# Kernel tuning notes

Measured on AMD Instinct MI355X. Metric: run time of the kernel, lower is better.

The kernel has to match this reference:

```python
import jax, jax.numpy as jnp
import numpy as np

SEQ_LEN, BATCH, HID, INP = 512, 256, 256, 256


def setup_inputs() -> dict:
    key = jax.random.key(0)
    ks = jax.random.split(key, 6)
    s = 1.0 / np.sqrt(HID)  # torch GRUCell init scale
    return {
        "carry": jnp.zeros((BATCH, HID), jnp.float32),
        "seq_inputs": jax.random.normal(ks[0], (SEQ_LEN, BATCH, INP), jnp.float32),
        "seq_resets": jax.random.randint(ks[1], (SEQ_LEN, BATCH), 0, 2, jnp.int32),
        "w_ih": jax.random.uniform(ks[2], (3 * HID, INP), jnp.float32, -s, s),
        "w_hh": jax.random.uniform(ks[3], (3 * HID, HID), jnp.float32, -s, s),
        "b_ih": jax.random.uniform(ks[4], (3 * HID,), jnp.float32, -s, s),
        "b_hh": jax.random.uniform(ks[5], (3 * HID,), jnp.float32, -s, s),
    }


def reference(carry, seq_inputs, seq_resets, w_ih, w_hh, b_ih, b_hh):
    # Precompute the input-side projection for all timesteps in one GEMM.
    gi_all = jnp.einsum('tbi,gi->tbg', seq_inputs, w_ih) + b_ih  # (T,B,3H)

    def step(h, xs):
        gi, reset_t = xs
        h = jnp.where(reset_t[:, None] > 0, jnp.zeros_like(h), h)
        gh = h @ w_hh.T + b_hh  # (B,3H)
        i_r, i_z, i_n = jnp.split(gi, 3, axis=1)
        h_r, h_z, h_n = jnp.split(gh, 3, axis=1)
        r = jax.nn.sigmoid(i_r + h_r)
        z = jax.nn.sigmoid(i_z + h_z)
        n = jnp.tanh(i_n + r * h_n)
        h_new = (1.0 - z) * n + z * h
        return h_new, h_new

    h_final, outputs = jax.lax.scan(step, carry, (gi_all, seq_resets))
    return h_final, outputs
```

## Files before the change

kernel.cpp:

```cpp
#include <hip/hip_runtime.h>
#include <hip/hip_bf16.h>
#include <hip/hip_fp16.h>


#define T_LEN 512
#define BATCH 256
#define HID   256

typedef __attribute__((ext_vector_type(8))) short s16x8;
typedef __attribute__((ext_vector_type(8))) unsigned short u16x8;
typedef __attribute__((ext_vector_type(4))) float fx4;

#define MFMA16 __builtin_amdgcn_mfma_f32_16x16x32_bf16
#define GATE_STRIDE 4096u
#define BLK_STRIDE  12288u
#define T_STRIDE    196608u

__device__ __forceinline__ unsigned short f2bf(float f) {
  union { float f; unsigned u; } v; v.f = f;
  unsigned r = v.u + 0x7fffu + ((v.u >> 16) & 1u);
  return (unsigned short)(r >> 16);
}

__device__ __forceinline__ unsigned cvt_pk_bf16(float lo, float hi) {
  unsigned r;
  asm("v_cvt_pk_bf16_f32 %0, %1, %2" : "=v"(r) : "v"(lo), "v"(hi));
  return r;
}

__device__ __forceinline__ s16x8 pack8(float4 a, float4 b) {
  s16x8 f;
  f[0] = (short)f2bf(a.x); f[1] = (short)f2bf(a.y);
  f[2] = (short)f2bf(a.z); f[3] = (short)f2bf(a.w);
  f[4] = (short)f2bf(b.x); f[5] = (short)f2bf(b.y);
  f[6] = (short)f2bf(b.z); f[7] = (short)f2bf(b.w);
  return f;
}

__device__ __forceinline__ s16x8 pack8i(float4 a, float4 b) {
  s16x8 f;
  f[0] = (short)f2bf(a.x); f[1] = (short)f2bf(b.x);
  f[2] = (short)f2bf(a.y); f[3] = (short)f2bf(b.y);
  f[4] = (short)f2bf(a.z); f[5] = (short)f2bf(b.z);
  f[6] = (short)f2bf(a.w); f[7] = (short)f2bf(b.w);
  return f;
}

template<bool SIGMA>
__device__ __forceinline__ void load_weights(const float* __restrict__ W,
                                             s16x8 (&wr)[4][8], char* Wlds,
                                             int tid, int wid, int col, int kgrp) {
#pragma unroll
  for (int g = 0; g < 2; ++g)
#pragma unroll
    for (int ht = 0; ht < 2; ++ht) {
      int row = g * 256 + (wid * 2 + ht) * 16 + col;
#pragma unroll
      for (int s8 = 0; s8 < 8; ++s8) {
        if (SIGMA) {
          const float* pa = W + row * 256 + s8 * 32 + kgrp * 4;
          wr[g * 2 + ht][s8] = pack8i(*(const float4*)pa, *(const float4*)(pa + 16));
        } else {
          const float* pa = W + row * 256 + s8 * 32 + kgrp * 8;
          wr[g * 2 + ht][s8] = pack8(*(const float4*)pa, *(const float4*)(pa + 4));
        }
      }
    }
#pragma unroll
  for (int q = 0; q < 16; ++q) {
    int li = tid + q * 512;
    int wv = li >> 9, s8 = (li >> 6) & 7, l = li & 63;
    int row = 512 + wv * 16 + (l & 15);
    s16x8 line;
    if (SIGMA) {
      const float* pa = W + row * 256 + s8 * 32 + (l >> 4) * 4;
      line = pack8i(*(const float4*)pa, *(const float4*)(pa + 16));
    } else {
      const float* pa = W + row * 256 + s8 * 32 + (l >> 4) * 8;
      line = pack8(*(const float4*)pa, *(const float4*)(pa + 4));
    }
    *(s16x8*)(Wlds + li * 16) = line;
  }
}

__device__ __forceinline__ void soft_barrier() {
  asm volatile("s_waitcnt lgkmcnt(0)" ::: "memory");
  __builtin_amdgcn_s_barrier();
  __builtin_amdgcn_sched_barrier(0);
  asm volatile("" ::: "memory");
}

__global__ __launch_bounds__(512, 2) void gi_proj_kernel(
    const float* __restrict__ X, const float* __restrict__ w_ih,
    const float* __restrict__ b_ih, const float* __restrict__ b_hh,
    __half* __restrict__ gi) {
  __shared__ __align__(16) char Wlds[131072];
  __shared__ __align__(16) char Ald[2][8192];

  const int tid = threadIdx.x;
  const int wid = tid >> 6, lane = tid & 63;
  const int col = lane & 15, kgrp = lane >> 4;

  s16x8 wr[4][8];
  load_weights<false>(w_ih, wr, Wlds, tid, wid, col, kgrp);

  float bias[2][3];
#pragma unroll
  for (int ht = 0; ht < 2; ++ht) {
    int gb = (wid * 2 + ht) * 16 + col;
    bias[ht][0] = b_ih[gb]       + b_hh[gb];
    bias[ht][1] = b_ih[256 + gb] + b_hh[256 + gb];
    bias[ht][2] = b_ih[512 + gb];
  }

  const int srow = tid >> 5, sk = (tid & 31) * 8;
  const unsigned sbyte = ((unsigned)(srow * 512 + sk * 2)) ^ ((unsigned)(srow & 7) << 4);

  float4 xc0 = *(const float4*)(X + (size_t)(blockIdx.x * 16 + srow) * 256 + sk);
  float4 xc1 = *(const float4*)(X + (size_t)(blockIdx.x * 16 + srow) * 256 + sk + 4);

  int parity = 0;
  for (int chunk = blockIdx.x; chunk < (T_LEN * BATCH) / 16; chunk += 256) {
    char* ab = Ald[parity];
    {
      uint4 v;
      v.x = cvt_pk_bf16(xc0.x, xc0.y);
      v.y = cvt_pk_bf16(xc0.z, xc0.w);
      v.z = cvt_pk_bf16(xc1.x, xc1.y);
      v.w = cvt_pk_bf16(xc1.z, xc1.w);
      *(uint4*)(ab + sbyte) = v;
    }
    int nchunk = chunk + 256;
    if (nchunk < (T_LEN * BATCH) / 16) {
      xc0 = *(const float4*)(X + (size_t)(nchunk * 16 + srow) * 256 + sk);
      xc1 = *(const float4*)(X + (size_t)(nchunk * 16 + srow) * 256 + sk + 4);
    }
    soft_barrier();

    fx4 a00, a10, a01, a11, a02, a12;
#pragma unroll
    for (int j = 0; j < 4; ++j) {
      a00[j] = bias[0][0]; a10[j] = bias[1][0];
      a01[j] = bias[0][1]; a11[j] = bias[1][1];
      a02[j] = bias[0][2]; a12[j] = bias[1][2];
    }

#pragma unroll
    for (int s8 = 0; s8 < 8; ++s8) {
      unsigned aoff = ((unsigned)(col * 512 + (s8 * 32 + kgrp * 8) * 2)) ^
                      ((unsigned)(col & 7) << 4);
      s16x8 af  = *(const s16x8*)(ab + aoff);
      s16x8 w2a = *(const s16x8*)(Wlds + (((wid * 2 + 0) * 8 + s8) * 64 + lane) * 16);
      s16x8 w2b = *(const s16x8*)(Wlds + (((wid * 2 + 1) * 8 + s8) * 64 + lane) * 16);
      a00 = MFMA16(af, wr[0][s8], a00, 0, 0, 0);
      a10 = MFMA16(af, wr[1][s8], a10, 0, 0, 0);
      a01 = MFMA16(af, wr[2][s8], a01, 0, 0, 0);
      a11 = MFMA16(af, wr[3][s8], a11, 0, 0, 0);
      a02 = MFMA16(af, w2a, a02, 0, 0, 0);
      a12 = MFMA16(af, w2b, a12, 0, 0, 0);
    }

    __half* gb = gi + (size_t)chunk * BLK_STRIDE + (unsigned)(wid * 64 + lane) * 8;
    u16x8 o0, o1, o2;
#pragma unroll
    for (int j = 0; j < 4; ++j) {
      o0[j] = __half_as_ushort(__float2half(a00[j]));
      o0[4 + j] = __half_as_ushort(__float2half(a10[j]));
      o1[j] = __half_as_ushort(__float2half(a01[j]));
      o1[4 + j] = __half_as_ushort(__float2half(a11[j]));
      o2[j] = __half_as_ushort(__float2half(a02[j]));
      o2[4 + j] = __half_as_ushort(__float2half(a12[j]));
    }
    *(u16x8*)(gb) = o0;
    *(u16x8*)(gb + GATE_STRIDE) = o1;
    *(u16x8*)(gb + 2 * GATE_STRIDE) = o2;
    parity ^= 1;
  }
}

__global__ __launch_bounds__(512, 2) void gru_scan_kernel(
    const float* __restrict__ carry, const __half* __restrict__ gi,
    const int* __restrict__ resets, const float* __restrict__ w_hh,
    const float* __restrict__ b_hh, float* __restrict__ out) {
  __shared__ __align__(16) char Wlds[131072];
  __shared__ __align__(16) char Ald[2][8192];
  __shared__ int lastreset[16];

  const int tid = threadIdx.x;
  const int wid = tid >> 6, lane = tid & 63;
  const int col = lane & 15, kgrp = lane >> 4;
  const int bid = blockIdx.x;
  const int bt = bid & 15, c = bid >> 4;
  const int b0 = bt * 16, t0 = c * 32, t1 = t0 + 32;
  const int hid0 = wid * 32 + col;

  s16x8 wr[4][8];
  load_weights<true>(w_hh, wr, Wlds, tid, wid, col, kgrp);
  const float bhhn0 = b_hh[512 + hid0], bhhn1 = b_hh[512 + hid0 + 16];

  int s, useCarry;
  if (c == 0) {
    s = 0; useCarry = 1;
  } else {
    if (tid < 16) lastreset[tid] = -1;
    for (int base = t0 - 32;; base -= 32) {
      __syncthreads();
      int tt = base + (tid >> 4);
      if (tt >= 0 && tt < t0) {
        if (resets[tt * BATCH + b0 + (tid & 15)] != 0)
          atomicMax(&lastreset[tid & 15], tt);
      }
      __syncthreads();
      int mn = t0, all = 1;
#pragma unroll
      for (int i = 0; i < 16; ++i) {
        int v = lastreset[i];
        all &= (v >= 0) ? 1 : 0;
        mn = min(mn, v < 0 ? t0 : v);
      }
      if (all) { s = mn; useCarry = 0; break; }
      if (base <= 0) { s = 0; useCarry = 1; break; }
    }
  }

  {
    int row = tid >> 5, k0 = (tid & 31) * 8;
    int tile = k0 >> 5, colb = (k0 >> 1) & 15;
    int rst = resets[s * BATCH + b0 + row];
    float4 va = {0.f, 0.f, 0.f, 0.f}, vb = va;
    if (useCarry && !rst) {
      va = *(const float4*)(carry + (size_t)(b0 + row) * HID + tile * 32 + colb);
      vb = *(const float4*)(carry + (size_t)(b0 + row) * HID + tile * 32 + colb + 16);
    }
    uint4 u;
    u.x = cvt_pk_bf16(va.x, vb.x);
    u.y = cvt_pk_bf16(va.y, vb.y);
    u.z = cvt_pk_bf16(va.z, vb.z);
    u.w = cvt_pk_bf16(va.w, vb.w);
    unsigned byteoff = ((unsigned)(row * 512 + k0 * 2)) ^ ((unsigned)(row & 7) << 4);
    *(uint4*)(Ald[0] + byteoff) = u;
  }
  float hprev[2][4];
#pragma unroll
  for (int ht = 0; ht < 2; ++ht)
#pragma unroll
    for (int j = 0; j < 4; ++j) {
      int b = kgrp * 4 + j;
      int rst = resets[s * BATCH + b0 + b];
      float hv = 0.f;
      if (useCarry && !rst) hv = carry[(size_t)(b0 + b) * HID + hid0 + ht * 16];
      hprev[ht][j] = hv;
    }
  __syncthreads();

  const __half* gp = gi + (size_t)(s * 16 + bt) * BLK_STRIDE + (unsigned)(wid * 64 + lane) * 8;
  const int* rbase = resets + b0 + kgrp * 4;
  float* opc = out + 65536 + ((size_t)s * BATCH + b0 + kgrp * 4) * HID + hid0;

  u16x8 gP0 = *(const u16x8*)(gp);
  u16x8 gP1 = *(const u16x8*)(gp + GATE_STRIDE);
  u16x8 gP2 = *(const u16x8*)(gp + 2 * GATE_STRIDE);
  int4 rnC = *(const int4*)(rbase + (size_t)((s + 1 < T_LEN) ? s + 1 : T_LEN - 1) * BATCH);

  for (int t = s; t < t1; ++t) {
    const __half* gq = gp + ((t + 1 < t1) ? T_STRIDE : 0u);
    u16x8 gN0 = *(const u16x8*)(gq);
    u16x8 gN1 = *(const u16x8*)(gq + GATE_STRIDE);
    u16x8 gN2 = *(const u16x8*)(gq + 2 * GATE_STRIDE);
    int tn = (t + 2 < T_LEN) ? t + 2 : T_LEN - 1;
    int4 rnN = *(const int4*)(rbase + (size_t)tn * BATCH);

    fx4 a00, a10, a01, a11, a02, a12;
#pragma unroll
    for (int j = 0; j < 4; ++j) {
      a00[j] = __half2float(__ushort_as_half(gP0[j]));
      a10[j] = __half2float(__ushort_as_half(gP0[4 + j]));
      a01[j] = __half2float(__ushort_as_half(gP1[j]));
      a11[j] = __half2float(__ushort_as_half(gP1[4 + j]));
      a02[j] = bhhn0;
      a12[j] = bhhn1;
    }

    const char* ab = Ald[(t - s) & 1];
#pragma unroll
    for (int s8 = 0; s8 < 8; ++s8) {
      unsigned aoff = ((unsigned)(col * 512 + (s8 * 32 + kgrp * 8) * 2)) ^
                      ((unsigned)(col & 7) << 4);
      s16x8 af  = *(const s16x8*)(ab + aoff);
      s16x8 w2a = *(const s16x8*)(Wlds + (((wid * 2 + 0) * 8 + s8) * 64 + lane) * 16);
      s16x8 w2b = *(const s16x8*)(Wlds + (((wid * 2 + 1) * 8 + s8) * 64 + lane) * 16);
      a00 = MFMA16(af, wr[0][s8], a00, 0, 0, 0);
      a10 = MFMA16(af, wr[1][s8], a10, 0, 0, 0);
      a01 = MFMA16(af, wr[2][s8], a01, 0, 0, 0);
      a11 = MFMA16(af, wr[3][s8], a11, 0, 0, 0);
      a02 = MFMA16(af, w2a, a02, 0, 0, 0);
      a12 = MFMA16(af, w2b, a12, 0, 0, 0);
    }

    char* aw = (char*)Ald[((t - s) & 1) ^ 1];
    const bool wr_out = (t >= t0);
    const bool lastT = (t + 1 >= T_LEN);
#pragma unroll
    for (int j = 0; j < 4; ++j) {
      int b = kgrp * 4 + j;
      int rj = (j == 0) ? rnC.x : (j == 1) ? rnC.y : (j == 2) ? rnC.z : rnC.w;
      if (lastT) rj = 0;

      float r0 = __builtin_amdgcn_rcpf(1.f + __expf(-a00[j]));
      float z0 = __builtin_amdgcn_rcpf(1.f + __expf(-a01[j]));
      float pn0 = __half2float(__ushort_as_half(gP2[j])) + r0 * a02[j];
      float n0 = 1.f - 2.f * __builtin_amdgcn_rcpf(1.f + __expf(2.f * pn0));
      float h0 = (1.f - z0) * n0 + z0 * hprev[0][j];

      float r1 = __builtin_amdgcn_rcpf(1.f + __expf(-a10[j]));
      float z1 = __builtin_amdgcn_rcpf(1.f + __expf(-a11[j]));
      float pn1 = __half2float(__ushort_as_half(gP2[4 + j])) + r1 * a12[j];
      float n1 = 1.f - 2.f * __builtin_amdgcn_rcpf(1.f + __expf(2.f * pn1));
      float h1 = (1.f - z1) * n1 + z1 * hprev[1][j];

      if (wr_out) {
        __builtin_nontemporal_store(h0, opc + j * HID);
        __builtin_nontemporal_store(h1, opc + j * HID + 16);
      }

      float hk0 = rj ? 0.f : h0;
      float hk1 = rj ? 0.f : h1;
      hprev[0][j] = hk0; hprev[1][j] = hk1;

      unsigned hw = cvt_pk_bf16(hk0, hk1);
      unsigned hoff = ((unsigned)(b * 512 + wid * 64 + col * 4)) ^
                      ((unsigned)(b & 7) << 4);
      *(unsigned*)(aw + hoff) = hw;
    }

    gP0 = gN0; gP1 = gN1; gP2 = gN2; rnC = rnN;
    gp = gq;
    opc += 65536;
    soft_barrier();
  }

  if (c == 15) {
#pragma unroll
    for (int ht = 0; ht < 2; ++ht)
#pragma unroll
      for (int j = 0; j < 4; ++j)
        out[(size_t)(b0 + kgrp * 4 + j) * HID + hid0 + ht * 16] = hprev[ht][j];
  }
}

extern "C" void kernel_launch(void* const* d_in, const int* in_sizes, int n_in,
                              void* d_out, int out_size, void* d_ws, size_t ws_size,
                              hipStream_t stream) {
  const float* carry = (const float*)d_in[0];
  const float* X     = (const float*)d_in[1];
  const int*   rsts  = (const int*)d_in[2];
  const float* w_ih  = (const float*)d_in[3];
  const float* w_hh  = (const float*)d_in[4];
  const float* b_ih  = (const float*)d_in[5];
  const float* b_hh  = (const float*)d_in[6];
  float* out = (float*)d_out;

  const size_t gi_bytes = (size_t)T_LEN * BATCH * 3 * HID * sizeof(__half);
  if (ws_size < gi_bytes) return;
  __half* gi = (__half*)d_ws;

  gi_proj_kernel<<<256, 512, 0, stream>>>(X, w_ih, b_ih, b_hh, gi);
  gru_scan_kernel<<<256, 512, 0, stream>>>(carry, gi, rsts, w_hh, b_hh, out);
}
```

Baseline: 247.3 us.

## Process 32 batch rows per block with 16-step chunks and interleaved gate layout

Each GRU scan block now covers 32 batch rows (two M-tiles) over 16-step time chunks instead of 16 rows over 32 steps. That keeps the block count the same while each weight fragment loaded from registers and LDS feeds twice as many MFMAs. The gi projection layout is changed to interleave r/z/n per lane, giving contiguous 48-half loads, and the projection kernel is tiled to match. Shorter chunks reduce the redundant warm-up recompute before each chunk start. The cost is more register pressure (doubled accumulators and prefetched gates) and a larger LDS activation buffer.

```diff
diff --git a/kernel.cpp b/kernel.cpp
--- a/kernel.cpp
+++ b/kernel.cpp
@@ -6,15 +6,15 @@
 #define T_LEN 512
 #define BATCH 256
 #define HID   256
+#define CHL   16
 
 typedef __attribute__((ext_vector_type(8))) short s16x8;
 typedef __attribute__((ext_vector_type(8))) unsigned short u16x8;
 typedef __attribute__((ext_vector_type(4))) float fx4;
 
 #define MFMA16 __builtin_amdgcn_mfma_f32_16x16x32_bf16
-#define GATE_STRIDE 4096u
-#define BLK_STRIDE  12288u
-#define T_STRIDE    196608u
+#define BLKH  24576u
+#define TSTRH 196608u
 
 __device__ __forceinline__ unsigned short f2bf(float f) {
   union { float f; unsigned u; } v; v.f = f;
@@ -48,29 +48,28 @@
 
 template<bool SIGMA>
 __device__ __forceinline__ void load_weights(const float* __restrict__ W,
-                                             s16x8 (&wr)[4][8], char* Wlds,
+                                             s16x8 (&wrA)[4][8], char* Wlds,
                                              int tid, int wid, int col, int kgrp) {
-#pragma unroll
-  for (int g = 0; g < 2; ++g)
-#pragma unroll
-    for (int ht = 0; ht < 2; ++ht) {
-      int row = g * 256 + (wid * 2 + ht) * 16 + col;
-#pragma unroll
-      for (int s8 = 0; s8 < 8; ++s8) {
-        if (SIGMA) {
-          const float* pa = W + row * 256 + s8 * 32 + kgrp * 4;
-          wr[g * 2 + ht][s8] = pack8i(*(const float4*)pa, *(const float4*)(pa + 16));
-        } else {
-          const float* pa = W + row * 256 + s8 * 32 + kgrp * 8;
-          wr[g * 2 + ht][s8] = pack8(*(const float4*)pa, *(const float4*)(pa + 4));
-        }
-      }
-    }
+  const int rowbase[4] = {0, 16, 256, 512};
+#pragma unroll
+  for (int k = 0; k < 4; ++k) {
+    int row = rowbase[k] + wid * 32 + col;
+#pragma unroll
+    for (int s8 = 0; s8 < 8; ++s8) {
+      if (SIGMA) {
+        const float* pa = W + row * 256 + s8 * 32 + kgrp * 4;
+        wrA[k][s8] = pack8i(*(const float4*)pa, *(const float4*)(pa + 16));
+      } else {
+        const float* pa = W + row * 256 + s8 * 32 + kgrp * 8;
+        wrA[k][s8] = pack8(*(const float4*)pa, *(const float4*)(pa + 4));
+      }
+    }
+  }
 #pragma unroll
   for (int q = 0; q < 16; ++q) {
     int li = tid + q * 512;
-    int wv = li >> 9, s8 = (li >> 6) & 7, l = li & 63;
-    int row = 512 + wv * 16 + (l & 15);
+    int set = li >> 12, wv = (li >> 9) & 7, s8 = (li >> 6) & 7, l = li & 63;
+    int row = (set ? 512 : 256) + wv * 32 + 16 + (l & 15);
     s16x8 line;
     if (SIGMA) {
       const float* pa = W + row * 256 + s8 * 32 + (l >> 4) * 4;
@@ -95,85 +94,93 @@
     const float* __restrict__ b_ih, const float* __restrict__ b_hh,
     __half* __restrict__ gi) {
   __shared__ __align__(16) char Wlds[131072];
-  __shared__ __align__(16) char Ald[2][8192];
+  __shared__ __align__(16) char Ald[2][16384];
 
   const int tid = threadIdx.x;
   const int wid = tid >> 6, lane = tid & 63;
   const int col = lane & 15, kgrp = lane >> 4;
 
-  s16x8 wr[4][8];
-  load_weights<false>(w_ih, wr, Wlds, tid, wid, col, kgrp);
+  s16x8 wrA[4][8];
+  load_weights<false>(w_ih, wrA, Wlds, tid, wid, col, kgrp);
 
   float bias[2][3];
 #pragma unroll
   for (int ht = 0; ht < 2; ++ht) {
-    int gb = (wid * 2 + ht) * 16 + col;
+    int gb = wid * 32 + ht * 16 + col;
     bias[ht][0] = b_ih[gb]       + b_hh[gb];
     bias[ht][1] = b_ih[256 + gb] + b_hh[256 + gb];
     bias[ht][2] = b_ih[512 + gb];
   }
 
-  const int srow = tid >> 5, sk = (tid & 31) * 8;
-  const unsigned sbyte = ((unsigned)(srow * 512 + sk * 2)) ^ ((unsigned)(srow & 7) << 4);
-
-  float4 xc0 = *(const float4*)(X + (size_t)(blockIdx.x * 16 + srow) * 256 + sk);
-  float4 xc1 = *(const float4*)(X + (size_t)(blockIdx.x * 16 + srow) * 256 + sk + 4);
+  const int srow = tid >> 4, skb = tid & 15;
+  const unsigned sx = (unsigned)(srow & 7) << 4;
+  const unsigned sb0 = (unsigned)(srow * 512 + skb * 32);
+
+  float4 xc0, xc1, xc2, xc3;
+  {
+    const float* xp = X + (size_t)(blockIdx.x * 32 + srow) * 256 + skb * 16;
+    xc0 = *(const float4*)(xp); xc1 = *(const float4*)(xp + 4);
+    xc2 = *(const float4*)(xp + 8); xc3 = *(const float4*)(xp + 12);
+  }
 
   int parity = 0;
-  for (int chunk = blockIdx.x; chunk < (T_LEN * BATCH) / 16; chunk += 256) {
+  for (int c32 = blockIdx.x; c32 < 4096; c32 += 256) {
     char* ab = Ald[parity];
     {
-      uint4 v;
-      v.x = cvt_pk_bf16(xc0.x, xc0.y);
-      v.y = cvt_pk_bf16(xc0.z, xc0.w);
-      v.z = cvt_pk_bf16(xc1.x, xc1.y);
-      v.w = cvt_pk_bf16(xc1.z, xc1.w);
-      *(uint4*)(ab + sbyte) = v;
-    }
-    int nchunk = chunk + 256;
-    if (nchunk < (T_LEN * BATCH) / 16) {
-      xc0 = *(const float4*)(X + (size_t)(nchunk * 16 + srow) * 256 + sk);
-      xc1 = *(const float4*)(X + (size_t)(nchunk * 16 + srow) * 256 + sk + 4);
+      uint4 u0, u1;
+      u0.x = cvt_pk_bf16(xc0.x, xc0.y); u0.y = cvt_pk_bf16(xc0.z, xc0.w);
+      u0.z = cvt_pk_bf16(xc1.x, xc1.y); u0.w = cvt_pk_bf16(xc1.z, xc1.w);
+      u1.x = cvt_pk_bf16(xc2.x, xc2.y); u1.y = cvt_pk_bf16(xc2.z, xc2.w);
+      u1.z = cvt_pk_bf16(xc3.x, xc3.y); u1.w = cvt_pk_bf16(xc3.z, xc3.w);
+      *(uint4*)(ab + (sb0 ^ sx)) = u0;
+      *(uint4*)(ab + ((sb0 + 16) ^ sx)) = u1;
+    }
+    int nc = c32 + 256;
+    if (nc < 4096) {
+      const float* xp = X + (size_t)(nc * 32 + srow) * 256 + skb * 16;
+      xc0 = *(const float4*)(xp); xc1 = *(const float4*)(xp + 4);
+      xc2 = *(const float4*)(xp + 8); xc3 = *(const float4*)(xp + 12);
     }
     soft_barrier();
 
-    fx4 a00, a10, a01, a11, a02, a12;
-#pragma unroll
-    for (int j = 0; j < 4; ++j) {
-      a00[j] = bias[0][0]; a10[j] = bias[1][0];
-      a01[j] = bias[0][1]; a11[j] = bias[1][1];
-      a02[j] = bias[0][2]; a12[j] = bias[1][2];
-    }
-
-#pragma unroll
-    for (int s8 = 0; s8 < 8; ++s8) {
-      unsigned aoff = ((unsigned)(col * 512 + (s8 * 32 + kgrp * 8) * 2)) ^
-                      ((unsigned)(col & 7) << 4);
-      s16x8 af  = *(const s16x8*)(ab + aoff);
-      s16x8 w2a = *(const s16x8*)(Wlds + (((wid * 2 + 0) * 8 + s8) * 64 + lane) * 16);
-      s16x8 w2b = *(const s16x8*)(Wlds + (((wid * 2 + 1) * 8 + s8) * 64 + lane) * 16);
-      a00 = MFMA16(af, wr[0][s8], a00, 0, 0, 0);
-      a10 = MFMA16(af, wr[1][s8], a10, 0, 0, 0);
-      a01 = MFMA16(af, wr[2][s8], a01, 0, 0, 0);
-      a11 = MFMA16(af, wr[3][s8], a11, 0, 0, 0);
-      a02 = MFMA16(af, w2a, a02, 0, 0, 0);
-      a12 = MFMA16(af, w2b, a12, 0, 0, 0);
-    }
-
-    __half* gb = gi + (size_t)chunk * BLK_STRIDE + (unsigned)(wid * 64 + lane) * 8;
-    u16x8 o0, o1, o2;
-#pragma unroll
-    for (int j = 0; j < 4; ++j) {
-      o0[j] = __half_as_ushort(__float2half(a00[j]));
-      o0[4 + j] = __half_as_ushort(__float2half(a10[j]));
-      o1[j] = __half_as_ushort(__float2half(a01[j]));
-      o1[4 + j] = __half_as_ushort(__float2half(a11[j]));
-      o2[j] = __half_as_ushort(__float2half(a02[j]));
-      o2[4 + j] = __half_as_ushort(__float2half(a12[j]));
-    }
-    *(u16x8*)(gb) = o0;
-    *(u16x8*)(gb + GATE_STRIDE) = o1;
-    *(u16x8*)(gb + 2 * GATE_STRIDE) = o2;
+    __half* gb = gi + (size_t)c32 * BLKH + (unsigned)(wid * 64 + lane) * 48;
+#pragma unroll
+    for (int m = 0; m < 2; ++m) {
+      fx4 aR0, aR1, aZ0, aZ1, aN0, aN1;
+#pragma unroll
+      for (int j = 0; j < 4; ++j) {
+        aR0[j] = bias[0][0]; aR1[j] = bias[1][0];
+        aZ0[j] = bias[0][1]; aZ1[j] = bias[1][1];
+        aN0[j] = bias[0][2]; aN1[j] = bias[1][2];
+      }
+#pragma unroll
+      for (int s8 = 0; s8 < 8; ++s8) {
+        unsigned aoff = ((unsigned)((m * 16 + col) * 512 + s8 * 64 + kgrp * 16)) ^
+                        ((unsigned)(col & 7) << 4);
+        s16x8 af  = *(const s16x8*)(ab + aoff);
+        s16x8 wz1 = *(const s16x8*)(Wlds + (wid * 512 + s8 * 64 + lane) * 16);
+        s16x8 wn1 = *(const s16x8*)(Wlds + 65536 + (wid * 512 + s8 * 64 + lane) * 16);
+        aR0 = MFMA16(af, wrA[0][s8], aR0, 0, 0, 0);
+        aR1 = MFMA16(af, wrA[1][s8], aR1, 0, 0, 0);
+        aZ0 = MFMA16(af, wrA[2][s8], aZ0, 0, 0, 0);
+        aZ1 = MFMA16(af, wz1, aZ1, 0, 0, 0);
+        aN0 = MFMA16(af, wrA[3][s8], aN0, 0, 0, 0);
+        aN1 = MFMA16(af, wn1, aN1, 0, 0, 0);
+      }
+      u16x8 oR, oZ, oN;
+#pragma unroll
+      for (int j = 0; j < 4; ++j) {
+        oR[j] = __half_as_ushort(__float2half(aR0[j]));
+        oR[4 + j] = __half_as_ushort(__float2half(aR1[j]));
+        oZ[j] = __half_as_ushort(__float2half(aZ0[j]));
+        oZ[4 + j] = __half_as_ushort(__float2half(aZ1[j]));
+        oN[j] = __half_as_ushort(__float2half(aN0[j]));
+        oN[4 + j] = __half_as_ushort(__float2half(aN1[j]));
+      }
+      *(u16x8*)(gb + m * 8) = oR;
+      *(u16x8*)(gb + 16 + m * 8) = oZ;
+      *(u16x8*)(gb + 32 + m * 8) = oN;
+    }
     parity ^= 1;
   }
 }
@@ -183,37 +190,37 @@
     const int* __restrict__ resets, const float* __restrict__ w_hh,
     const float* __restrict__ b_hh, float* __restrict__ out) {
   __shared__ __align__(16) char Wlds[131072];
-  __shared__ __align__(16) char Ald[2][8192];
-  __shared__ int lastreset[16];
+  __shared__ __align__(16) char Ald[2][16384];
+  int* lastreset = (int*)(Ald[1]);
 
   const int tid = threadIdx.x;
   const int wid = tid >> 6, lane = tid & 63;
   const int col = lane & 15, kgrp = lane >> 4;
   const int bid = blockIdx.x;
-  const int bt = bid & 15, c = bid >> 4;
-  const int b0 = bt * 16, t0 = c * 32, t1 = t0 + 32;
+  const int bt = bid & 7, c = bid >> 3;
+  const int b0 = bt * 32, t0 = c * CHL, t1 = t0 + CHL;
   const int hid0 = wid * 32 + col;
 
-  s16x8 wr[4][8];
-  load_weights<true>(w_hh, wr, Wlds, tid, wid, col, kgrp);
+  s16x8 wrA[4][8];
+  load_weights<true>(w_hh, wrA, Wlds, tid, wid, col, kgrp);
   const float bhhn0 = b_hh[512 + hid0], bhhn1 = b_hh[512 + hid0 + 16];
 
   int s, useCarry;
   if (c == 0) {
     s = 0; useCarry = 1;
   } else {
-    if (tid < 16) lastreset[tid] = -1;
-    for (int base = t0 - 32;; base -= 32) {
+    if (tid < 32) lastreset[tid] = -1;
+    for (int base = t0 - 16;; base -= 16) {
       __syncthreads();
-      int tt = base + (tid >> 4);
+      int tt = base + (tid >> 5);
       if (tt >= 0 && tt < t0) {
-        if (resets[tt * BATCH + b0 + (tid & 15)] != 0)
-          atomicMax(&lastreset[tid & 15], tt);
+        if (resets[tt * BATCH + b0 + (tid & 31)] != 0)
+          atomicMax(&lastreset[tid & 31], tt);
       }
       __syncthreads();
       int mn = t0, all = 1;
 #pragma unroll
-      for (int i = 0; i < 16; ++i) {
+      for (int i = 0; i < 32; ++i) {
         int v = lastreset[i];
         all &= (v >= 0) ? 1 : 0;
         mn = min(mn, v < 0 ? t0 : v);
@@ -221,130 +228,160 @@
       if (all) { s = mn; useCarry = 0; break; }
       if (base <= 0) { s = 0; useCarry = 1; break; }
     }
+    __syncthreads();
   }
 
   {
-    int row = tid >> 5, k0 = (tid & 31) * 8;
-    int tile = k0 >> 5, colb = (k0 >> 1) & 15;
+    int row = tid >> 4, kblk = tid & 15;
     int rst = resets[s * BATCH + b0 + row];
-    float4 va = {0.f, 0.f, 0.f, 0.f}, vb = va;
+    float4 va0 = {0.f, 0.f, 0.f, 0.f}, va1 = va0, vb0 = va0, vb1 = va0;
     if (useCarry && !rst) {
-      va = *(const float4*)(carry + (size_t)(b0 + row) * HID + tile * 32 + colb);
-      vb = *(const float4*)(carry + (size_t)(b0 + row) * HID + tile * 32 + colb + 16);
-    }
-    uint4 u;
-    u.x = cvt_pk_bf16(va.x, vb.x);
-    u.y = cvt_pk_bf16(va.y, vb.y);
-    u.z = cvt_pk_bf16(va.z, vb.z);
-    u.w = cvt_pk_bf16(va.w, vb.w);
-    unsigned byteoff = ((unsigned)(row * 512 + k0 * 2)) ^ ((unsigned)(row & 7) << 4);
-    *(uint4*)(Ald[0] + byteoff) = u;
-  }
-  float hprev[2][4];
-#pragma unroll
-  for (int ht = 0; ht < 2; ++ht)
+      const float* cp = carry + (size_t)(b0 + row) * HID + (kblk >> 1) * 32 + (kblk & 1) * 8;
+      va0 = *(const float4*)(cp);      va1 = *(const float4*)(cp + 4);
+      vb0 = *(const float4*)(cp + 16); vb1 = *(const float4*)(cp + 20);
+    }
+    uint4 u0, u1;
+    u0.x = cvt_pk_bf16(va0.x, vb0.x); u0.y = cvt_pk_bf16(va0.y, vb0.y);
+    u0.z = cvt_pk_bf16(va0.z, vb0.z); u0.w = cvt_pk_bf16(va0.w, vb0.w);
+    u1.x = cvt_pk_bf16(va1.x, vb1.x); u1.y = cvt_pk_bf16(va1.y, vb1.y);
+    u1.z = cvt_pk_bf16(va1.z, vb1.z); u1.w = cvt_pk_bf16(va1.w, vb1.w);
+    unsigned sx = (unsigned)(row & 7) << 4;
+    unsigned sb0 = (unsigned)(row * 512 + kblk * 32);
+    *(uint4*)(Ald[0] + (sb0 ^ sx)) = u0;
+    *(uint4*)(Ald[0] + ((sb0 + 16) ^ sx)) = u1;
+  }
+  float hprev[2][2][4];
+#pragma unroll
+  for (int m = 0; m < 2; ++m)
 #pragma unroll
     for (int j = 0; j < 4; ++j) {
-      int b = kgrp * 4 + j;
-      int rst = resets[s * BATCH + b0 + b];
-      float hv = 0.f;
-      if (useCarry && !rst) hv = carry[(size_t)(b0 + b) * HID + hid0 + ht * 16];
-      hprev[ht][j] = hv;
-    }
+      int b = b0 + m * 16 + kgrp * 4 + j;
+      int rst = resets[s * BATCH + b];
+      float h0 = 0.f, h1 = 0.f;
+      if (useCarry && !rst) {
+        h0 = carry[(size_t)b * HID + hid0];
+        h1 = carry[(size_t)b * HID + hid0 + 16];
+      }
+      hprev[m][0][j] = h0; hprev[m][1][j] = h1;
+    }
+
+  const __half* gb = gi + (size_t)(s * 8 + bt) * BLKH + (unsigned)(wid * 64 + lane) * 48;
+  u16x8 gC[3][2];
+#pragma unroll
+  for (int g = 0; g < 3; ++g)
+#pragma unroll
+    for (int m = 0; m < 2; ++m)
+      gC[g][m] = *(const u16x8*)(gb + g * 16 + m * 8);
+  int4 rnC[2];
+  {
+    int tn = (s + 1 < T_LEN) ? s + 1 : T_LEN - 1;
+#pragma unroll
+    for (int m = 0; m < 2; ++m)
+      rnC[m] = *(const int4*)(resets + (size_t)tn * BATCH + b0 + m * 16 + kgrp * 4);
+  }
+  float* opc = out + 65536 + ((size_t)s * BATCH + b0 + kgrp * 4) * HID + hid0;
   __syncthreads();
 
-  const __half* gp = gi + (size_t)(s * 16 + bt) * BLK_STRIDE + (unsigned)(wid * 64 + lane) * 8;
-  const int* rbase = resets + b0 + kgrp * 4;
-  float* opc = out + 65536 + ((size_t)s * BATCH + b0 + kgrp * 4) * HID + hid0;
-
-  u16x8 gP0 = *(const u16x8*)(gp);
-  u16x8 gP1 = *(const u16x8*)(gp + GATE_STRIDE);
-  u16x8 gP2 = *(const u16x8*)(gp + 2 * GATE_STRIDE);
-  int4 rnC = *(const int4*)(rbase + (size_t)((s + 1 < T_LEN) ? s + 1 : T_LEN - 1) * BATCH);
-
   for (int t = s; t < t1; ++t) {
-    const __half* gq = gp + ((t + 1 < t1) ? T_STRIDE : 0u);
-    u16x8 gN0 = *(const u16x8*)(gq);
-    u16x8 gN1 = *(const u16x8*)(gq + GATE_STRIDE);
-    u16x8 gN2 = *(const u16x8*)(gq + 2 * GATE_STRIDE);
-    int tn = (t + 2 < T_LEN) ? t + 2 : T_LEN - 1;
-    int4 rnN = *(const int4*)(rbase + (size_t)tn * BATCH);
-
-    fx4 a00, a10, a01, a11, a02, a12;
-#pragma unroll
-    for (int j = 0; j < 4; ++j) {
-      a00[j] = __half2float(__ushort_as_half(gP0[j]));
-      a10[j] = __half2float(__ushort_as_half(gP0[4 + j]));
-      a01[j] = __half2float(__ushort_as_half(gP1[j]));
-      a11[j] = __half2float(__ushort_as_half(gP1[4 + j]));
-      a02[j] = bhhn0;
-      a12[j] = bhhn1;
+    const __half* gq = gb + ((t + 1 < t1) ? TSTRH : 0u);
+    u16x8 gN[3][2];
+#pragma unroll
+    for (int g = 0; g < 3; ++g)
+#pragma unroll
+      for (int m = 0; m < 2; ++m)
+        gN[g][m] = *(const u16x8*)(gq + g * 16 + m * 8);
+    int4 rnN[2];
+    {
+      int tn = (t + 2 < T_LEN) ? t + 2 : T_LEN - 1;
+#pragma unroll
+      for (int m = 0; m < 2; ++m)
+        rnN[m] = *(const int4*)(resets + (size_t)tn * BATCH + b0 + m * 16 + kgrp * 4);
     }
 
     const char* ab = Ald[(t - s) & 1];
-#pragma unroll
-    for (int s8 = 0; s8 < 8; ++s8) {
-      unsigned aoff = ((unsigned)(col * 512 + (s8 * 32 + kgrp * 8) * 2)) ^
-                      ((unsigned)(col & 7) << 4);
-      s16x8 af  = *(const s16x8*)(ab + aoff);
-      s16x8 w2a = *(const s16x8*)(Wlds + (((wid * 2 + 0) * 8 + s8) * 64 + lane) * 16);
-      s16x8 w2b = *(const s16x8*)(Wlds + (((wid * 2 + 1) * 8 + s8) * 64 + lane) * 16);
-      a00 = MFMA16(af, wr[0][s8], a00, 0, 0, 0);
-      a10 = MFMA16(af, wr[1][s8], a10, 0, 0, 0);
-      a01 = MFMA16(af, wr[2][s8], a01, 0, 0, 0);
-      a11 = MFMA16(af, wr[3][s8], a11, 0, 0, 0);
-      a02 = MFMA16(af, w2a, a02, 0, 0, 0);
-      a12 = MFMA16(af, w2b, a12, 0, 0, 0);
-    }
-
     char* aw = (char*)Ald[((t - s) & 1) ^ 1];
-    const bool wr_out = (t >= t0);
     const bool lastT = (t + 1 >= T_LEN);
-#pragma unroll
-    for (int j = 0; j < 4; ++j) {
-      int b = kgrp * 4 + j;
-      int rj = (j == 0) ? rnC.x : (j == 1) ? rnC.y : (j == 2) ? rnC.z : rnC.w;
-      if (lastT) rj = 0;
-
-      float r0 = __builtin_amdgcn_rcpf(1.f + __expf(-a00[j]));
-      float z0 = __builtin_amdgcn_rcpf(1.f + __expf(-a01[j]));
-      float pn0 = __half2float(__ushort_as_half(gP2[j])) + r0 * a02[j];
-      float n0 = 1.f - 2.f * __builtin_amdgcn_rcpf(1.f + __expf(2.f * pn0));
-      float h0 = (1.f - z0) * n0 + z0 * hprev[0][j];
-
-      float r1 = __builtin_amdgcn_rcpf(1.f + __expf(-a10[j]));
-      float z1 = __builtin_amdgcn_rcpf(1.f + __expf(-a11[j]));
-      float pn1 = __half2float(__ushort_as_half(gP2[4 + j])) + r1 * a12[j];
-      float n1 = 1.f - 2.f * __builtin_amdgcn_rcpf(1.f + __expf(2.f * pn1));
-      float h1 = (1.f - z1) * n1 + z1 * hprev[1][j];
-
-      if (wr_out) {
-        __builtin_nontemporal_store(h0, opc + j * HID);
-        __builtin_nontemporal_store(h1, opc + j * HID + 16);
-      }
-
-      float hk0 = rj ? 0.f : h0;
-      float hk1 = rj ? 0.f : h1;
-      hprev[0][j] = hk0; hprev[1][j] = hk1;
-
-      unsigned hw = cvt_pk_bf16(hk0, hk1);
-      unsigned hoff = ((unsigned)(b * 512 + wid * 64 + col * 4)) ^
-                      ((unsigned)(b & 7) << 4);
-      *(unsigned*)(aw + hoff) = hw;
-    }
-
-    gP0 = gN0; gP1 = gN1; gP2 = gN2; rnC = rnN;
-    gp = gq;
+
+#pragma unroll
+    for (int m = 0; m < 2; ++m) {
+      fx4 aR0, aR1, aZ0, aZ1, aN0, aN1;
+#pragma unroll
+      for (int j = 0; j < 4; ++j) {
+        aR0[j] = __half2float(__ushort_as_half(gC[0][m][j]));
+        aR1[j] = __half2float(__ushort_as_half(gC[0][m][4 + j]));
+        aZ0[j] = __half2float(__ushort_as_half(gC[1][m][j]));
+        aZ1[j] = __half2float(__ushort_as_half(gC[1][m][4 + j]));
+        aN0[j] = bhhn0;
+        aN1[j] = bhhn1;
+      }
+#pragma unroll
+      for (int s8 = 0; s8 < 8; ++s8) {
+        unsigned aoff = ((unsigned)((m * 16 + col) * 512 + s8 * 64 + kgrp * 16)) ^
+                        ((unsigned)(col & 7) << 4);
+        s16x8 af  = *(const s16x8*)(ab + aoff);
+        s16x8 wz1 = *(const s16x8*)(Wlds + (wid * 512 + s8 * 64 + lane) * 16);
+        s16x8 wn1 = *(const s16x8*)(Wlds + 65536 + (wid * 512 + s8 * 64 + lane) * 16);
+        aR0 = MFMA16(af, wrA[0][s8], aR0, 0, 0, 0);
+        aR1 = MFMA16(af, wrA[1][s8], aR1, 0, 0, 0);
+        aZ0 = MFMA16(af, wrA[2][s8], aZ0, 0, 0, 0);
+        aZ1 = MFMA16(af, wz1, aZ1, 0, 0, 0);
+        aN0 = MFMA16(af, wrA[3][s8], aN0, 0, 0, 0);
+        aN1 = MFMA16(af, wn1, aN1, 0, 0, 0);
+      }
+
+      int4 rm = rnC[m];
+#pragma unroll
+      for (int j = 0; j < 4; ++j) {
+        int b = m * 16 + kgrp * 4 + j;
+        int rj = (j == 0) ? rm.x : (j == 1) ? rm.y : (j == 2) ? rm.z : rm.w;
+        if (lastT) rj = 0;
+
+        float r0 = __builtin_amdgcn_rcpf(1.f + __expf(-aR0[j]));
+        float z0 = __builtin_amdgcn_rcpf(1.f + __expf(-aZ0[j]));
+        float pn0 = __half2float(__ushort_as_half(gC[2][m][j])) + r0 * aN0[j];
+        float n0 = 1.f - 2.f * __builtin_amdgcn_rcpf(1.f + __expf(2.f * pn0));
+        float h0 = (1.f - z0) * n0 + z0 * hprev[m][0][j];
+
+        float r1 = __builtin_amdgcn_rcpf(1.f + __expf(-aR1[j]));
+        float z1 = __builtin_amdgcn_rcpf(1.f + __expf(-aZ1[j]));
+        float pn1 = __half2float(__ushort_as_half(gC[2][m][4 + j])) + r1 * aN1[j];
+        float n1 = 1.f - 2.f * __builtin_amdgcn_rcpf(1.f + __expf(2.f * pn1));
+        float h1 = (1.f - z1) * n1 + z1 * hprev[m][1][j];
+
+        __builtin_nontemporal_store(h0, opc + m * 4096 + j * HID);
+        __builtin_nontemporal_store(h1, opc + m * 4096 + j * HID + 16);
+
+        float hk0 = rj ? 0.f : h0;
+        float hk1 = rj ? 0.f : h1;
+        hprev[m][0][j] = hk0; hprev[m][1][j] = hk1;
+
+        unsigned hw = cvt_pk_bf16(hk0, hk1);
+        unsigned hoff = ((unsigned)(b * 512 + wid * 64 + col * 4)) ^
+                        ((unsigned)(b & 7) << 4);
+        *(unsigned*)(aw + hoff) = hw;
+      }
+    }
+
+#pragma unroll
+    for (int g = 0; g < 3; ++g)
+#pragma unroll
+      for (int m = 0; m < 2; ++m)
+        gC[g][m] = gN[g][m];
+    rnC[0] = rnN[0]; rnC[1] = rnN[1];
+    gb = gq;
     opc += 65536;
     soft_barrier();
   }
 
-  if (c == 15) {
-#pragma unroll
-    for (int ht = 0; ht < 2; ++ht)
-#pragma unroll
-      for (int j = 0; j < 4; ++j)
-        out[(size_t)(b0 + kgrp * 4 + j) * HID + hid0 + ht * 16] = hprev[ht][j];
+  if (c == 31) {
+#pragma unroll
+    for (int m = 0; m < 2; ++m)
+#pragma unroll
+      for (int j = 0; j < 4; ++j) {
+        int b = b0 + m * 16 + kgrp * 4 + j;
+        out[(size_t)b * HID + hid0] = hprev[m][0][j];
+        out[(size_t)b * HID + hid0 + 16] = hprev[m][1][j];
+      }
   }
 }
 
```

Result: slower. 348.2 us (+40.8%).
